# Kernel optimization log

Measured on AMD Instinct MI355X. Metric: run time of the kernel, lower is better.

The kernel has to match this reference:

```python
import jax, jax.numpy as jnp
import numpy as np

CODEBOOK_SLOTS = 1024
CODEBOOK_DIM = 256
TEMPERATURE = 0.5
BS, W = 32, 2048


def setup_inputs() -> dict:
    key = jax.random.key(0)
    k1, k2, k3 = jax.random.split(key, 3)
    z_e = jax.random.normal(k1, (BS, CODEBOOK_DIM, W), dtype=jnp.float32)
    codebook = jax.random.normal(k2, (CODEBOOK_SLOTS, CODEBOOK_DIM), dtype=jnp.float32)
    gumbel = jax.random.gumbel(k3, (BS * W, CODEBOOK_SLOTS), dtype=jnp.float32)
    return {"z_e": z_e, "codebook": codebook, "gumbel": gumbel}


def reference(z_e, codebook, gumbel):
    bs, feat_dim, w = z_e.shape
    slots = codebook.shape[0]
    log_slots_const = jnp.float32(np.log(slots))
    # (bs, feat_dim, w) -> (bs*w, feat_dim)
    z_flat = jnp.transpose(z_e, (0, 2, 1)).reshape(bs * w, feat_dim)
    # squared-distance matrix: ||z||^2 + ||c||^2 - 2 z.c  -> (bs*w, slots)
    cb_sqr = jnp.sum(codebook ** 2, axis=1)                 # (slots,)
    z_sqr = jnp.sum(z_flat ** 2, axis=1, keepdims=True)     # (bs*w, 1)
    distances = cb_sqr[None, :] + z_sqr - 2.0 * (z_flat @ codebook.T)
    logits = -distances
    # RelaxedOneHotCategorical.rsample: softmax((logits + gumbel)/tau)
    soft_onehot = jax.nn.softmax((logits + gumbel) / TEMPERATURE, axis=1)
    hard_indices = jnp.argmax(soft_onehot, axis=1).reshape(bs, w)
    # weighted codebook lookup -> (bs, feat_dim, w)
    z_q = (soft_onehot @ codebook).reshape(bs, w, feat_dim)
    z_q = jnp.transpose(z_q, (0, 2, 1))
    # dist.probs = softmax(logits)
    probs = jax.nn.softmax(logits, axis=1)
    kl = (probs * (jnp.log(probs + 1e-9) + log_slots_const))
    kl = kl.reshape(bs, w, slots).sum(axis=(1, 2)).mean()
    commit_loss = (probs * distances).reshape(bs, w, slots).sum(axis=(1, 2)).mean()
    return z_q, hard_indices, kl, commit_loss
```

## Files before the change

kernel.cpp:

```cpp
#include <hip/hip_runtime.h>

#define BSZ 32
#define DIMD 256
#define WW 2048
#define SLOTS 1024
#define NROWS (BSZ*WW)
#define LOG_SLOTS 6.931471805599453f
#define THR 4.0f

#define ZQ_N (BSZ*DIMD*WW)
#define IDX_OFF ZQ_N
#define KL_OFF (ZQ_N + NROWS)
#define CM_OFF (KL_OFF + 1)

#define WS_CH   0u
#define WS_CL   524288u
#define WS_PV   1048576u
#define WS_CBSQ 1572864u
#define WS_TOP  1576960u
#define WS_MR   2625536u
#define WS_NORM 11014144u
#define WS_U    11538432u
#define WS_NEED 145756160ull

typedef _Float16 half2_t __attribute__((ext_vector_type(2)));
typedef _Float16 half8_t __attribute__((ext_vector_type(8)));
typedef float v4f __attribute__((ext_vector_type(4)));

__device__ __forceinline__ void pmerge(float& m, float& s, float& t, float om, float os, float ot) {
  float M = fmaxf(m, om);
  float ea = __expf(m - M), eb = __expf(om - M);
  s = s * ea + os * eb;
  t = t * ea + ot * eb;
  m = M;
}

__device__ __forceinline__ void top3_merge(float& v1, float& i1, float& v2, float& i2, float& v3,
                                           float ov1, float oi1, float ov2, float oi2, float ov3) {
  bool sw = (ov1 > v1) || (ov1 == v1 && oi1 < i1);
  float a1v = sw ? ov1 : v1, a1i = sw ? oi1 : i1;
  float a2v = sw ? ov2 : v2, a2i = sw ? oi2 : i2;
  float a3v = sw ? ov3 : v3;
  float b1v = sw ? v1 : ov1, b1i = sw ? i1 : oi1;
  float b2v = sw ? v2 : ov2;
  bool a2w = (a2v > b1v) || (a2v == b1v && a2i < b1i);
  v1 = a1v; i1 = a1i;
  v2 = a2w ? a2v : b1v;
  i2 = a2w ? a2i : b1i;
  v3 = a2w ? fmaxf(a3v, b1v) : fmaxf(a2v, b2v);
}

__global__ void k0_zero(float* out) { out[KL_OFF] = 0.f; out[CM_OFF] = 0.f; }

__global__ void k2_pack(const float* __restrict__ cb, _Float16* __restrict__ chs,
                        _Float16* __restrict__ cls, _Float16* __restrict__ pvs,
                        float* __restrict__ cbsq) {
  const int tid = blockIdx.x * 256 + threadIdx.x;
  if (tid < 32768) {
    const int lane = tid & 63;
    {
      const int ks = (tid >> 6) & 7, sblk = tid >> 9;
      const int col = sblk * 16 + (lane & 15);
      const int k0 = ks * 32 + (lane >> 4) * 8;
      half8_t vh, vl;
#pragma unroll
      for (int j = 0; j < 8; ++j) {
        const float v = cb[(size_t)col * DIMD + k0 + j];
        const _Float16 h = (_Float16)v;
        vh[j] = h;
        vl[j] = (_Float16)(v - (float)h);
      }
      *(half8_t*)&chs[(size_t)tid * 8] = vh;
      *(half8_t*)&cls[(size_t)tid * 8] = vl;
    }
    {
      const int idx = tid >> 6;
      const int cf = idx >> 4, dt = idx & 15;
      const int d = dt * 16 + (lane & 15);
      const int s0 = cf * 32 + (lane >> 4) * 8;
      half8_t vp;
#pragma unroll
      for (int j = 0; j < 8; ++j)
        vp[j] = (_Float16)cb[(size_t)(s0 + j) * DIMD + d];
      *(half8_t*)&pvs[(size_t)tid * 8] = vp;
    }
  }
  if (tid < SLOTS) {
    double a = 0.0;
    for (int i = 0; i < DIMD; ++i) { const double v = (double)cb[(size_t)tid * DIMD + i]; a += v * v; }
    cbsq[tid] = (float)a;
  }
}

__device__ __forceinline__ void stage_chunk(const _Float16* __restrict__ chs,
                                            const _Float16* __restrict__ cls,
                                            _Float16* bsh, _Float16* bsl,
                                            int cf, int wv, int lane) {
  const size_t gbase = (size_t)cf * 8192 + wv * 2048 + lane * 8;
#pragma unroll
  for (int i = 0; i < 4; ++i) {
    __builtin_amdgcn_global_load_lds(
        (const __attribute__((address_space(1))) void*)(chs + gbase + i * 512),
        (__attribute__((address_space(3))) void*)(bsh + wv * 2048 + i * 512), 16, 0, 0);
    __builtin_amdgcn_global_load_lds(
        (const __attribute__((address_space(1))) void*)(cls + gbase + i * 512),
        (__attribute__((address_space(3))) void*)(bsl + wv * 2048 + i * 512), 16, 0, 0);
  }
}

__global__ __launch_bounds__(256) __attribute__((amdgpu_waves_per_eu(2)))
void k3_main(const float* __restrict__ z_e, const float* __restrict__ gum,
             const _Float16* __restrict__ chs, const _Float16* __restrict__ cls,
             const float* __restrict__ cbsq, _Float16* __restrict__ ubig,
             float* __restrict__ mrbuf, float2* __restrict__ normbuf,
             float* __restrict__ topw, float* __restrict__ out) {
  __shared__ _Float16 bsh[8192];
  __shared__ _Float16 bsl[8192];
  __shared__ _Float16 ubuf[4][16][44];

  const int t = threadIdx.x, wv = t >> 6, lane = t & 63, l15 = lane & 15, lq = lane >> 4;
  const int r0 = blockIdx.x * 64;
  const int rw = r0 + wv * 16;
  const int rt = blockIdx.x * 4 + wv;
  const int b = r0 >> 11;
  const int w0 = rw & 2047;
  const int ph = ((blockIdx.x >> 8) & 1) << 4;

  stage_chunk(chs, cls, bsh, bsl, ph, wv, lane);

  const float* zbase = z_e + (size_t)b * DIMD * WW + w0 + l15;
  half8_t ah[8], al[8];
  float zacc = 0.f;
#pragma unroll
  for (int ks = 0; ks < 8; ++ks) {
#pragma unroll
    for (int j = 0; j < 8; ++j) {
      const float v = zbase[(size_t)(ks * 32 + lq * 8 + j) * WW];
      zacc += v * v;
      const _Float16 h = (_Float16)v;
      ah[ks][j] = h;
      al[ks][j] = (_Float16)(v - (float)h);
    }
  }
  zacc += __shfl_xor(zacc, 16);
  zacc += __shfl_xor(zacc, 32);
  float zs[4];
#pragma unroll
  for (int g = 0; g < 4; ++g) zs[g] = __shfl(zacc, lq * 4 + g);

  float m1[4], s1[4], t1[4], v1[4], v2[4], v3[4], i1[4], i2[4], s2[4], mr[4];
#pragma unroll
  for (int g = 0; g < 4; ++g) {
    m1[g] = -1e30f; s1[g] = 0.f; t1[g] = 0.f;
    v1[g] = -1e30f; v2[g] = -1e30f; v3[g] = -1e30f; i1[g] = 0.f; i2[g] = 0.f;
    s2[g] = 0.f; mr[g] = -1e30f;
  }

  const float* gbase = gum + (size_t)rw * SLOTS;
  float gc[8], cbc[2];
#pragma unroll
  for (int c = 0; c < 2; ++c) {
    cbc[c] = cbsq[ph * 32 + c * 16 + l15];
#pragma unroll
    for (int g = 0; g < 4; ++g)
      gc[c * 4 + g] = gbase[(size_t)(lq * 4 + g) * SLOTS + ph * 32 + c * 16 + l15];
  }

  __syncthreads();

#pragma unroll 1
  for (int cf = 0; cf < 32; ++cf) {
    const int cfa = (cf + ph) & 31;
    const int cfn = (cfa + 1) & 31;
    float gn[8], cbn[2];
    if (cf < 31) {
#pragma unroll
      for (int c = 0; c < 2; ++c) {
        cbn[c] = cbsq[cfn * 32 + c * 16 + l15];
#pragma unroll
        for (int g = 0; g < 4; ++g)
          gn[c * 4 + g] = gbase[(size_t)(lq * 4 + g) * SLOTS + cfn * 32 + c * 16 + l15];
      }
    }
    v4f qh[2], ql[2];
    qh[0] = v4f{0.f, 0.f, 0.f, 0.f}; qh[1] = v4f{0.f, 0.f, 0.f, 0.f};
    ql[0] = v4f{0.f, 0.f, 0.f, 0.f}; ql[1] = v4f{0.f, 0.f, 0.f, 0.f};
#pragma unroll
    for (int ks = 0; ks < 8; ++ks) {
      const int o0 = ((0 * 8 + ks) * 64 + lane) * 8;
      const int o1 = ((1 * 8 + ks) * 64 + lane) * 8;
      const half8_t bh0 = *(const half8_t*)&bsh[o0];
      const half8_t bl0 = *(const half8_t*)&bsl[o0];
      const half8_t bh1 = *(const half8_t*)&bsh[o1];
      const half8_t bl1 = *(const half8_t*)&bsl[o1];
      qh[0] = __builtin_amdgcn_mfma_f32_16x16x32_f16(ah[ks], bh0, qh[0], 0, 0, 0);
      ql[0] = __builtin_amdgcn_mfma_f32_16x16x32_f16(al[ks], bh0, ql[0], 0, 0, 0);
      ql[0] = __builtin_amdgcn_mfma_f32_16x16x32_f16(ah[ks], bl0, ql[0], 0, 0, 0);
      qh[1] = __builtin_amdgcn_mfma_f32_16x16x32_f16(ah[ks], bh1, qh[1], 0, 0, 0);
      ql[1] = __builtin_amdgcn_mfma_f32_16x16x32_f16(al[ks], bh1, ql[1], 0, 0, 0);
      ql[1] = __builtin_amdgcn_mfma_f32_16x16x32_f16(ah[ks], bl1, ql[1], 0, 0, 0);
    }
    __syncthreads();
    if (cf < 31) stage_chunk(chs, cls, bsh, bsl, cfn, wv, lane);

    float yv[8];
#pragma unroll
    for (int c = 0; c < 2; ++c) {
      const int col = cfa * 32 + c * 16 + l15;
      const float cq = cbc[c];
      const float fc = (float)col;
#pragma unroll
      for (int g = 0; g < 4; ++g) {
        const float dd = cq + zs[g] - 2.f * (qh[c][g] + ql[c][g]);
        const float lv = -dd;
        if (__builtin_expect(lv > m1[g] + 8.f, 0)) {
          const float f = __expf(m1[g] - lv);
          s1[g] *= f; t1[g] *= f; m1[g] = lv;
        }
        const float e = __expf(lv - m1[g]);
        s1[g] += e;
        t1[g] = __fmaf_rn(e, dd, t1[g]);
        const float y = __fmaf_rn(-2.f, dd, 2.f * gc[c * 4 + g]);
        yv[c * 4 + g] = y;
        if (__builtin_expect(y > v3[g], 0)) {
          const bool b1 = (y > v1[g]);
          const bool b2 = (y > v2[g]);
          v3[g] = b2 ? v2[g] : y;
          v2[g] = b1 ? v1[g] : (b2 ? y : v2[g]);
          i2[g] = b1 ? i1[g] : (b2 ? fc : i2[g]);
          v1[g] = b1 ? y : v1[g];
          i1[g] = b1 ? fc : i1[g];
        }
      }
    }
#pragma unroll
    for (int g = 0; g < 4; ++g) {
      if (__builtin_expect(__any(v1[g] > mr[g] + THR), 0)) {
        float vm = v1[g];
#pragma unroll
        for (int mk = 1; mk < 16; mk <<= 1) vm = fmaxf(vm, __shfl_xor(vm, mk));
        if (vm > mr[g] + THR) {
          s2[g] *= __expf(mr[g] - vm);
          mr[g] = vm;
        }
      }
    }
#pragma unroll
    for (int c = 0; c < 2; ++c)
#pragma unroll
      for (int g = 0; g < 4; ++g) {
        const float u = __expf(yv[c * 4 + g] - mr[g]);
        s2[g] += u;
        ubuf[wv][lq * 4 + g][c * 16 + l15] = (_Float16)u;
      }
    if (l15 == 0) {
#pragma unroll
      for (int g = 0; g < 4; ++g)
        mrbuf[((size_t)rt * 32 + cfa) * 16 + lq * 4 + g] = mr[g];
    }
    const half8_t pa = *(const half8_t*)&ubuf[wv][l15][lq * 8];
    *(half8_t*)&ubig[((size_t)rt * 32 + cfa) * 512 + l15 * 32 + lq * 8] = pa;
    if (cf < 31) {
#pragma unroll
      for (int i = 0; i < 8; ++i) gc[i] = gn[i];
      cbc[0] = cbn[0]; cbc[1] = cbn[1];
    }
    __syncthreads();
  }

#pragma unroll
  for (int mk = 1; mk < 16; mk <<= 1) {
#pragma unroll
    for (int g = 0; g < 4; ++g) {
      const float om = __shfl_xor(m1[g], mk);
      const float os = __shfl_xor(s1[g], mk);
      const float ot = __shfl_xor(t1[g], mk);
      pmerge(m1[g], s1[g], t1[g], om, os, ot);
      const float ov1 = __shfl_xor(v1[g], mk);
      const float oi1 = __shfl_xor(i1[g], mk);
      const float ov2 = __shfl_xor(v2[g], mk);
      const float oi2 = __shfl_xor(i2[g], mk);
      const float ov3 = __shfl_xor(v3[g], mk);
      top3_merge(v1[g], i1[g], v2[g], i2[g], v3[g], ov1, oi1, ov2, oi2, ov3);
      s2[g] += __shfl_xor(s2[g], mk);
    }
  }
  float klsum = 0.f, cmsum = 0.f;
#pragma unroll
  for (int g = 0; g < 4; ++g) {
    const float commit_row = t1[g] / s1[g];
    const float lse = m1[g] + logf(s1[g]);
    klsum += -commit_row - lse + LOG_SLOTS;
    cmsum += commit_row;
    if (l15 == 0) {
      const int row = rw + lq * 4 + g;
      out[IDX_OFF + row] = i1[g];
      float4 tv; tv.x = v1[g]; tv.y = v2[g]; tv.z = v3[g]; tv.w = i2[g];
      *(float4*)&topw[(size_t)row * 4] = tv;
      normbuf[row] = make_float2(mr[g], 1.f / s2[g]);
    }
  }
  float kw = (l15 == 0) ? klsum : 0.f;
  float cw = (l15 == 0) ? cmsum : 0.f;
#pragma unroll
  for (int mk = 1; mk < 64; mk <<= 1) { kw += __shfl_xor(kw, mk); cw += __shfl_xor(cw, mk); }
  if (lane == 0) {
    atomicAdd(&out[KL_OFF], kw * 0.03125f);
    atomicAdd(&out[CM_OFF], cw * 0.03125f);
  }
}

__global__ __launch_bounds__(256) __attribute__((amdgpu_waves_per_eu(2)))
void k4_pv(const _Float16* __restrict__ ubig, const float* __restrict__ mrbuf,
           const float2* __restrict__ normbuf, const _Float16* __restrict__ pvs,
           float* __restrict__ out) {
  const int t = threadIdx.x, wv = t >> 6, lane = t & 63, l15 = lane & 15, lq = lane >> 4;
  const int rt = blockIdx.x * 4 + wv;
  const int r0 = rt * 16;
  const int b = r0 >> 11, w0 = r0 & 2047;
  const float2 nv = normbuf[r0 + l15];
  const float mrfin = nv.x, inv = nv.y;
  v4f pacc[16];
#pragma unroll
  for (int dt = 0; dt < 16; ++dt) pacc[dt] = v4f{0.f, 0.f, 0.f, 0.f};

  float mrc = mrbuf[(size_t)rt * 32 * 16 + l15];
  half8_t pa0 = *(const half8_t*)&ubig[(size_t)rt * 32 * 512 + l15 * 32 + lq * 8];
#pragma unroll 1
  for (int cf = 0; cf < 32; ++cf) {
    float mrn = 0.f; half8_t pan = pa0;
    if (cf < 31) {
      mrn = mrbuf[((size_t)rt * 32 + cf + 1) * 16 + l15];
      pan = *(const half8_t*)&ubig[((size_t)rt * 32 + cf + 1) * 512 + l15 * 32 + lq * 8];
    }
    const float f = __expf(mrc - mrfin);
    half8_t pa;
#pragma unroll
    for (int j = 0; j < 8; ++j) pa[j] = (_Float16)((float)pa0[j] * f);
#pragma unroll
    for (int dt = 0; dt < 16; ++dt) {
      const half8_t pb = *(const half8_t*)&pvs[((size_t)(cf * 16 + dt) * 64 + lane) * 8];
      pacc[dt] = __builtin_amdgcn_mfma_f32_16x16x32_f16(pb, pa, pacc[dt], 0, 0, 0);
    }
    mrc = mrn; pa0 = pan;
  }
#pragma unroll
  for (int dt = 0; dt < 16; ++dt)
#pragma unroll
    for (int g = 0; g < 4; ++g)
      out[((size_t)b * DIMD + dt * 16 + lq * 4 + g) * WW + w0 + l15] = pacc[dt][g] * inv;
}

__global__ void k5_repair(const float* __restrict__ z_e, const float* __restrict__ cb,
                          const float* __restrict__ gum, const float* __restrict__ topw,
                          float* __restrict__ out) {
  const int wv = threadIdx.x >> 6, lane = threadIdx.x & 63;
#pragma unroll 1
  for (int rr = 0; rr < 64; ++rr) {
    const int r = blockIdx.x * 256 + wv * 64 + rr;
    const float4 tw = *(const float4*)&topw[(size_t)r * 4];
    if (tw.x - tw.y >= 0.02f) continue;
    const int b = r >> 11, w = r & 2047;
    double zd[4]; double zq = 0.0;
#pragma unroll
    for (int i = 0; i < 4; ++i) {
      const float zz = z_e[((size_t)b * DIMD + lane + i * 64) * WW + w];
      zd[i] = (double)zz; zq += zd[i] * zd[i];
    }
#pragma unroll
    for (int mk = 1; mk < 64; mk <<= 1) zq += __shfl_xor(zq, mk);
    const int c1 = (int)out[IDX_OFF + r];
    const int c2 = (int)tw.w;
    const bool full = (tw.x - tw.z < 0.02f);
    double bestv = -1e300; int besti = 0;
    const int nc = full ? SLOTS : 2;
    for (int ci = 0; ci < nc; ++ci) {
      const int s = full ? ci : (ci == 0 ? c1 : c2);
      double dot = 0.0, csq = 0.0;
#pragma unroll
      for (int i = 0; i < 4; ++i) {
        const double cv = (double)cb[(size_t)s * DIMD + lane + i * 64];
        dot += zd[i] * cv; csq += cv * cv;
      }
#pragma unroll
      for (int mk = 1; mk < 64; mk <<= 1) { dot += __shfl_xor(dot, mk); csq += __shfl_xor(csq, mk); }
      const double y = 2.0 * ((double)gum[(size_t)r * SLOTS + s] - (csq + zq - 2.0 * dot));
      if (y > bestv || (y == bestv && s < besti)) { bestv = y; besti = s; }
    }
    if (lane == 0) out[IDX_OFF + r] = (float)besti;
  }
}

extern "C" void kernel_launch(void* const* d_in, const int* in_sizes, int n_in,
                              void* d_out, int out_size, void* d_ws, size_t ws_size,
                              hipStream_t stream) {
  const float* z_e = (const float*)d_in[0];
  const float* cb  = (const float*)d_in[1];
  const float* gum = (const float*)d_in[2];
  float* out = (float*)d_out;
  char* ws = (char*)d_ws;
  if (ws_size < WS_NEED) {
    hipMemsetAsync(d_out, 0, (size_t)out_size * sizeof(float), stream);
    return;
  }
  _Float16* chs = (_Float16*)(ws + WS_CH);
  _Float16* cls = (_Float16*)(ws + WS_CL);
  _Float16* pvs = (_Float16*)(ws + WS_PV);
  float* cbsq = (float*)(ws + WS_CBSQ);
  float* topw = (float*)(ws + WS_TOP);
  float* mrbuf = (float*)(ws + WS_MR);
  float2* normbuf = (float2*)(ws + WS_NORM);
  _Float16* ubig = (_Float16*)(ws + WS_U);
  k0_zero<<<1, 1, 0, stream>>>(out);
  k2_pack<<<128, 256, 0, stream>>>(cb, chs, cls, pvs, cbsq);
  k3_main<<<1024, 256, 0, stream>>>(z_e, gum, chs, cls, cbsq, ubig, mrbuf, normbuf, topw, out);
  k4_pv<<<1024, 256, 0, stream>>>(ubig, mrbuf, normbuf, pvs, out);
  k5_repair<<<256, 256, 0, stream>>>(z_e, cb, gum, topw, out);
}
```

Measured before the change: 461.7 us.

## Process two codebook chunks per iteration to halve barriers

The main loop now stages and computes two 32-slot codebook chunks per iteration (16 iterations instead of 32), doubling the LDS staging buffers and the u-buffer. This halves the number of block barriers and staging rounds and gives more independent MFMA chains per iteration. It also drops the per-block phase offset that staggered which chunk blocks start on, so all blocks now read the same codebook chunks at once. In exchange it doubles LDS use (about 64KB+) and raises register pressure from the larger gumbel prefetch and accumulator sets, which may lower occupancy.

```diff
diff --git a/kernel.cpp b/kernel.cpp
--- a/kernel.cpp
+++ b/kernel.cpp
@@ -114,9 +114,9 @@
              const float* __restrict__ cbsq, _Float16* __restrict__ ubig,
              float* __restrict__ mrbuf, float2* __restrict__ normbuf,
              float* __restrict__ topw, float* __restrict__ out) {
-  __shared__ _Float16 bsh[8192];
-  __shared__ _Float16 bsl[8192];
-  __shared__ _Float16 ubuf[4][16][44];
+  __shared__ _Float16 bsh[2][8192];
+  __shared__ _Float16 bsl[2][8192];
+  __shared__ _Float16 ubuf[2][4][16][44];
 
   const int t = threadIdx.x, wv = t >> 6, lane = t & 63, l15 = lane & 15, lq = lane >> 4;
   const int r0 = blockIdx.x * 64;
@@ -124,9 +124,9 @@
   const int rt = blockIdx.x * 4 + wv;
   const int b = r0 >> 11;
   const int w0 = rw & 2047;
-  const int ph = ((blockIdx.x >> 8) & 1) << 4;
-
-  stage_chunk(chs, cls, bsh, bsl, ph, wv, lane);
+
+  stage_chunk(chs, cls, bsh[0], bsl[0], 0, wv, lane);
+  stage_chunk(chs, cls, bsh[1], bsl[1], 1, wv, lane);
 
   const float* zbase = z_e + (size_t)b * DIMD * WW + w0 + l15;
   half8_t ah[8], al[8];
@@ -157,113 +157,132 @@
   }
 
   const float* gbase = gum + (size_t)rw * SLOTS;
-  float gc[8], cbc[2];
-#pragma unroll
-  for (int c = 0; c < 2; ++c) {
-    cbc[c] = cbsq[ph * 32 + c * 16 + l15];
-#pragma unroll
-    for (int g = 0; g < 4; ++g)
-      gc[c * 4 + g] = gbase[(size_t)(lq * 4 + g) * SLOTS + ph * 32 + c * 16 + l15];
-  }
+  float gc[16], cbc[4];
+#pragma unroll
+  for (int ch = 0; ch < 2; ++ch)
+#pragma unroll
+    for (int c = 0; c < 2; ++c) {
+      cbc[ch * 2 + c] = cbsq[ch * 32 + c * 16 + l15];
+#pragma unroll
+      for (int g = 0; g < 4; ++g)
+        gc[ch * 8 + c * 4 + g] = gbase[(size_t)(lq * 4 + g) * SLOTS + ch * 32 + c * 16 + l15];
+    }
 
   __syncthreads();
 
 #pragma unroll 1
-  for (int cf = 0; cf < 32; ++cf) {
-    const int cfa = (cf + ph) & 31;
-    const int cfn = (cfa + 1) & 31;
-    float gn[8], cbn[2];
-    if (cf < 31) {
+  for (int p = 0; p < 16; ++p) {
+    float gn[16], cbn[4];
+    if (p < 15) {
+#pragma unroll
+      for (int ch = 0; ch < 2; ++ch)
+#pragma unroll
+        for (int c = 0; c < 2; ++c) {
+          const int col0 = (p * 2 + 2 + ch) * 32 + c * 16 + l15;
+          cbn[ch * 2 + c] = cbsq[col0];
+#pragma unroll
+          for (int g = 0; g < 4; ++g)
+            gn[ch * 8 + c * 4 + g] = gbase[(size_t)(lq * 4 + g) * SLOTS + col0];
+        }
+    }
+    v4f qh[2][2], ql[2][2];
+#pragma unroll
+    for (int ch = 0; ch < 2; ++ch)
 #pragma unroll
       for (int c = 0; c < 2; ++c) {
-        cbn[c] = cbsq[cfn * 32 + c * 16 + l15];
+        qh[ch][c] = v4f{0.f, 0.f, 0.f, 0.f};
+        ql[ch][c] = v4f{0.f, 0.f, 0.f, 0.f};
+      }
+#pragma unroll
+    for (int ks = 0; ks < 8; ++ks) {
+#pragma unroll
+      for (int ch = 0; ch < 2; ++ch) {
+        const int o0 = ((0 * 8 + ks) * 64 + lane) * 8;
+        const int o1 = ((1 * 8 + ks) * 64 + lane) * 8;
+        const half8_t bh0 = *(const half8_t*)&bsh[ch][o0];
+        const half8_t bl0 = *(const half8_t*)&bsl[ch][o0];
+        const half8_t bh1 = *(const half8_t*)&bsh[ch][o1];
+        const half8_t bl1 = *(const half8_t*)&bsl[ch][o1];
+        qh[ch][0] = __builtin_amdgcn_mfma_f32_16x16x32_f16(ah[ks], bh0, qh[ch][0], 0, 0, 0);
+        ql[ch][0] = __builtin_amdgcn_mfma_f32_16x16x32_f16(al[ks], bh0, ql[ch][0], 0, 0, 0);
+        ql[ch][0] = __builtin_amdgcn_mfma_f32_16x16x32_f16(ah[ks], bl0, ql[ch][0], 0, 0, 0);
+        qh[ch][1] = __builtin_amdgcn_mfma_f32_16x16x32_f16(ah[ks], bh1, qh[ch][1], 0, 0, 0);
+        ql[ch][1] = __builtin_amdgcn_mfma_f32_16x16x32_f16(al[ks], bh1, ql[ch][1], 0, 0, 0);
+        ql[ch][1] = __builtin_amdgcn_mfma_f32_16x16x32_f16(ah[ks], bl1, ql[ch][1], 0, 0, 0);
+      }
+    }
+    __syncthreads();
+    if (p < 15) {
+      stage_chunk(chs, cls, bsh[0], bsl[0], p * 2 + 2, wv, lane);
+      stage_chunk(chs, cls, bsh[1], bsl[1], p * 2 + 3, wv, lane);
+    }
+
+#pragma unroll
+    for (int ch = 0; ch < 2; ++ch) {
+      const int cfa = p * 2 + ch;
+      float yv[8];
+#pragma unroll
+      for (int c = 0; c < 2; ++c) {
+        const int col = cfa * 32 + c * 16 + l15;
+        const float cq = cbc[ch * 2 + c];
+        const float fc = (float)col;
+#pragma unroll
+        for (int g = 0; g < 4; ++g) {
+          const float dd = cq + zs[g] - 2.f * (qh[ch][c][g] + ql[ch][c][g]);
+          const float lv = -dd;
+          if (__builtin_expect(lv > m1[g] + 8.f, 0)) {
+            const float f = __expf(m1[g] - lv);
+            s1[g] *= f; t1[g] *= f; m1[g] = lv;
+          }
+          const float e = __expf(lv - m1[g]);
+          s1[g] += e;
+          t1[g] = __fmaf_rn(e, dd, t1[g]);
+          const float y = __fmaf_rn(-2.f, dd, 2.f * gc[ch * 8 + c * 4 + g]);
+          yv[c * 4 + g] = y;
+          if (__builtin_expect(y > v3[g], 0)) {
+            const bool b1 = (y > v1[g]);
+            const bool b2 = (y > v2[g]);
+            v3[g] = b2 ? v2[g] : y;
+            v2[g] = b1 ? v1[g] : (b2 ? y : v2[g]);
+            i2[g] = b1 ? i1[g] : (b2 ? fc : i2[g]);
+            v1[g] = b1 ? y : v1[g];
+            i1[g] = b1 ? fc : i1[g];
+          }
+        }
+      }
+#pragma unroll
+      for (int g = 0; g < 4; ++g) {
+        if (__builtin_expect(__any(v1[g] > mr[g] + THR), 0)) {
+          float vm = v1[g];
+#pragma unroll
+          for (int mk = 1; mk < 16; mk <<= 1) vm = fmaxf(vm, __shfl_xor(vm, mk));
+          if (vm > mr[g] + THR) {
+            s2[g] *= __expf(mr[g] - vm);
+            mr[g] = vm;
+          }
+        }
+      }
+#pragma unroll
+      for (int c = 0; c < 2; ++c)
+#pragma unroll
+        for (int g = 0; g < 4; ++g) {
+          const float u = __expf(yv[c * 4 + g] - mr[g]);
+          s2[g] += u;
+          ubuf[ch][wv][lq * 4 + g][c * 16 + l15] = (_Float16)u;
+        }
+      if (l15 == 0) {
 #pragma unroll
         for (int g = 0; g < 4; ++g)
-          gn[c * 4 + g] = gbase[(size_t)(lq * 4 + g) * SLOTS + cfn * 32 + c * 16 + l15];
-      }
-    }
-    v4f qh[2], ql[2];
-    qh[0] = v4f{0.f, 0.f, 0.f, 0.f}; qh[1] = v4f{0.f, 0.f, 0.f, 0.f};
-    ql[0] = v4f{0.f, 0.f, 0.f, 0.f}; ql[1] = v4f{0.f, 0.f, 0.f, 0.f};
-#pragma unroll
-    for (int ks = 0; ks < 8; ++ks) {
-      const int o0 = ((0 * 8 + ks) * 64 + lane) * 8;
-      const int o1 = ((1 * 8 + ks) * 64 + lane) * 8;
-      const half8_t bh0 = *(const half8_t*)&bsh[o0];
-      const half8_t bl0 = *(const half8_t*)&bsl[o0];
-      const half8_t bh1 = *(const half8_t*)&bsh[o1];
-      const half8_t bl1 = *(const half8_t*)&bsl[o1];
-      qh[0] = __builtin_amdgcn_mfma_f32_16x16x32_f16(ah[ks], bh0, qh[0], 0, 0, 0);
-      ql[0] = __builtin_amdgcn_mfma_f32_16x16x32_f16(al[ks], bh0, ql[0], 0, 0, 0);
-      ql[0] = __builtin_amdgcn_mfma_f32_16x16x32_f16(ah[ks], bl0, ql[0], 0, 0, 0);
-      qh[1] = __builtin_amdgcn_mfma_f32_16x16x32_f16(ah[ks], bh1, qh[1], 0, 0, 0);
-      ql[1] = __builtin_amdgcn_mfma_f32_16x16x32_f16(al[ks], bh1, ql[1], 0, 0, 0);
-      ql[1] = __builtin_amdgcn_mfma_f32_16x16x32_f16(ah[ks], bl1, ql[1], 0, 0, 0);
-    }
-    __syncthreads();
-    if (cf < 31) stage_chunk(chs, cls, bsh, bsl, cfn, wv, lane);
-
-    float yv[8];
-#pragma unroll
-    for (int c = 0; c < 2; ++c) {
-      const int col = cfa * 32 + c * 16 + l15;
-      const float cq = cbc[c];
-      const float fc = (float)col;
-#pragma unroll
-      for (int g = 0; g < 4; ++g) {
-        const float dd = cq + zs[g] - 2.f * (qh[c][g] + ql[c][g]);
-        const float lv = -dd;
-        if (__builtin_expect(lv > m1[g] + 8.f, 0)) {
-          const float f = __expf(m1[g] - lv);
-          s1[g] *= f; t1[g] *= f; m1[g] = lv;
-        }
-        const float e = __expf(lv - m1[g]);
-        s1[g] += e;
-        t1[g] = __fmaf_rn(e, dd, t1[g]);
-        const float y = __fmaf_rn(-2.f, dd, 2.f * gc[c * 4 + g]);
-        yv[c * 4 + g] = y;
-        if (__builtin_expect(y > v3[g], 0)) {
-          const bool b1 = (y > v1[g]);
-          const bool b2 = (y > v2[g]);
-          v3[g] = b2 ? v2[g] : y;
-          v2[g] = b1 ? v1[g] : (b2 ? y : v2[g]);
-          i2[g] = b1 ? i1[g] : (b2 ? fc : i2[g]);
-          v1[g] = b1 ? y : v1[g];
-          i1[g] = b1 ? fc : i1[g];
-        }
-      }
-    }
-#pragma unroll
-    for (int g = 0; g < 4; ++g) {
-      if (__builtin_expect(__any(v1[g] > mr[g] + THR), 0)) {
-        float vm = v1[g];
-#pragma unroll
-        for (int mk = 1; mk < 16; mk <<= 1) vm = fmaxf(vm, __shfl_xor(vm, mk));
-        if (vm > mr[g] + THR) {
-          s2[g] *= __expf(mr[g] - vm);
-          mr[g] = vm;
-        }
-      }
-    }
-#pragma unroll
-    for (int c = 0; c < 2; ++c)
-#pragma unroll
-      for (int g = 0; g < 4; ++g) {
-        const float u = __expf(yv[c * 4 + g] - mr[g]);
-        s2[g] += u;
-        ubuf[wv][lq * 4 + g][c * 16 + l15] = (_Float16)u;
-      }
-    if (l15 == 0) {
-#pragma unroll
-      for (int g = 0; g < 4; ++g)
-        mrbuf[((size_t)rt * 32 + cfa) * 16 + lq * 4 + g] = mr[g];
-    }
-    const half8_t pa = *(const half8_t*)&ubuf[wv][l15][lq * 8];
-    *(half8_t*)&ubig[((size_t)rt * 32 + cfa) * 512 + l15 * 32 + lq * 8] = pa;
-    if (cf < 31) {
-#pragma unroll
-      for (int i = 0; i < 8; ++i) gc[i] = gn[i];
-      cbc[0] = cbn[0]; cbc[1] = cbn[1];
+          mrbuf[((size_t)rt * 32 + cfa) * 16 + lq * 4 + g] = mr[g];
+      }
+      const half8_t pa = *(const half8_t*)&ubuf[ch][wv][l15][lq * 8];
+      *(half8_t*)&ubig[((size_t)rt * 32 + cfa) * 512 + l15 * 32 + lq * 8] = pa;
+    }
+    if (p < 15) {
+#pragma unroll
+      for (int i = 0; i < 16; ++i) gc[i] = gn[i];
+#pragma unroll
+      for (int i = 0; i < 4; ++i) cbc[i] = cbn[i];
     }
     __syncthreads();
   }
```

Measured after the change: 477.5 us. 3.4% more time.
